# Kernel optimization log

Measured on AMD Instinct MI355X. Metric: run time of the kernel, lower is better.

The kernel has to match this reference:

```python
import jax, jax.numpy as jnp
import numpy as np

B, S, D_FF = 2, 2048, 1024
NUM_HEADS, D_KV = 16, 64
INNER = NUM_HEADS * D_KV


def setup_inputs() -> dict:
    key = jax.random.key(0)
    ks = jax.random.split(key, 8)
    scale = 1.0 / np.sqrt(D_FF)
    return {
        "q": jax.random.normal(ks[0], (B, S, D_FF), jnp.float32),
        "k": jax.random.normal(ks[1], (B, S, D_FF), jnp.float32),
        "v": jax.random.normal(ks[2], (B, S, D_FF), jnp.float32),
        "attn_mask": jax.random.normal(ks[3], (B, 1, S, S), jnp.float32),
        "Wq": jax.random.normal(ks[4], (INNER, D_FF), jnp.float32) * scale,
        "Wk": jax.random.normal(ks[5], (INNER, D_FF), jnp.float32) * scale,
        "Wv": jax.random.normal(ks[6], (INNER, D_FF), jnp.float32) * scale,
        "Wo": jax.random.normal(ks[7], (D_FF, INNER), jnp.float32) * scale,
        "num_heads": NUM_HEADS,
    }


def reference(q, k, v, attn_mask, Wq, Wk, Wv, Wo, num_heads):
    b, s, _ = q.shape
    # torch Linear (no bias): x @ W.T with W of shape [out, in]
    def proj_heads(x, W):
        y = jnp.einsum("bsd,ed->bse", x, W)  # [B,S,inner]
        return y.reshape(b, s, num_heads, -1).transpose(0, 2, 1, 3)  # [B,H,S,dk]

    qh = proj_heads(q, Wq)
    kh = proj_heads(k, Wk)
    vh = proj_heads(v, Wv)
    # T5 attention: NO 1/sqrt(d) scaling; additive mask bias before softmax
    scores = jnp.einsum("bhqd,bhkd->bhqk", qh, kh) + attn_mask  # [B,H,S,S]
    probs = jax.nn.softmax(scores, axis=-1)
    ctx = jnp.einsum("bhqk,bhkd->bhqd", probs, vh)  # [B,H,S,dk]
    ctx = ctx.transpose(0, 2, 1, 3).reshape(b, s, -1)  # [B,S,inner]
    return jnp.einsum("bse,de->bsd", ctx, Wo)  # [B,S,d_ff]
```

## Files before the change

### kernel.cpp

```cpp
#include <hip/hip_runtime.h>
#include <hip/hip_bf16.h>


typedef __attribute__((ext_vector_type(8))) short short8_t;
typedef __attribute__((ext_vector_type(4))) short short4_t;
typedef __attribute__((ext_vector_type(4))) float f32x4_t;

#define SEQ 2048
#define HEADS 16
#define DK 64
#define DFF 1024

__device__ __forceinline__ unsigned short f32_to_bf16(float f) {
  unsigned int u = __float_as_uint(f);
  u += 0x7FFFu + ((u >> 16) & 1u);
  return (unsigned short)(u >> 16);
}
__device__ __forceinline__ float bf16_to_f32(unsigned short h) {
  return __uint_as_float(((unsigned int)h) << 16);
}

__device__ __forceinline__ void gload_lds16(const void* g, void* l) {
  __builtin_amdgcn_global_load_lds(
      (__attribute__((address_space(1))) void*)(g),
      (__attribute__((address_space(3))) void*)(l), 16, 0, 0);
}

__global__ void cvt_x_kernel(const float* __restrict__ q,
                             const float* __restrict__ k,
                             const float* __restrict__ v,
                             short* __restrict__ dst, int n) {
  const float* src = (blockIdx.y == 0) ? q : (blockIdx.y == 1) ? k : v;
  short* out = dst + (size_t)blockIdx.y * n;
  int i = (blockIdx.x * 256 + threadIdx.x) * 4;
  if (i >= n) return;
  float4 f = *(const float4*)(src + i);
  short4_t s;
  s[0] = (short)f32_to_bf16(f.x);
  s[1] = (short)f32_to_bf16(f.y);
  s[2] = (short)f32_to_bf16(f.z);
  s[3] = (short)f32_to_bf16(f.w);
  *(short4_t*)(out + i) = s;
}

__global__ void cvt_w_kernel(const float* __restrict__ Wq,
                             const float* __restrict__ Wk,
                             const float* __restrict__ Wv,
                             const float* __restrict__ Wo,
                             short* __restrict__ wbase, int n) {
  int y = blockIdx.y;
  const float* src = (y == 0) ? Wq : (y == 1) ? Wk : (y == 2) ? Wv : Wo;
  int i = (blockIdx.x * 256 + threadIdx.x) * 4;
  if (i >= n) return;
  float4 f = *(const float4*)(src + i);
  float ff[4] = {f.x, f.y, f.z, f.w};
  if (y < 3) {
    short* hi = wbase + (size_t)(2 * y) * n;
    short* lo = wbase + (size_t)(2 * y + 1) * n;
    short4_t h, l;
#pragma unroll
    for (int j = 0; j < 4; ++j) {
      unsigned short hh = f32_to_bf16(ff[j]);
      h[j] = (short)hh;
      l[j] = (short)f32_to_bf16(ff[j] - bf16_to_f32(hh));
    }
    *(short4_t*)(hi + i) = h;
    *(short4_t*)(lo + i) = l;
  } else {
    short* out = wbase + (size_t)6 * n;
    short4_t s;
#pragma unroll
    for (int j = 0; j < 4; ++j) s[j] = (short)f32_to_bf16(ff[j]);
    *(short4_t*)(out + i) = s;
  }
}

template <int EPI>
__global__ __launch_bounds__(256, 2) void gemm_proj(
    const short* __restrict__ A, const short* __restrict__ Bh,
    const short* __restrict__ Bl, short* __restrict__ Ohi,
    short* __restrict__ Olo, int M, int K) {
  __shared__ short As[128 * 32];
  __shared__ short Bsh[64 * 32];
  __shared__ short Bsl[64 * 32];

  const int tid = threadIdx.x;
  const int w = tid >> 6, l = tid & 63, g = l >> 4, c = l & 15;
  const int wr = w >> 1, wc = w & 1;
  const int m0 = blockIdx.y * 128, n0 = blockIdx.x * 64;

  f32x4_t acc[4][2] = {};

  for (int k0 = 0; k0 < K; k0 += 32) {
#pragma unroll
    for (int j = 0; j < 2; ++j) {
      int e = (w * 2 + j) * 512 + l * 8;
      int r = e >> 5, cc = e & 31;
      gload_lds16(A + (size_t)(m0 + r) * K + k0 + cc, &As[(w * 2 + j) * 512]);
    }
    {
      int e = w * 512 + l * 8;
      int r = e >> 5, cc = e & 31;
      gload_lds16(Bh + (size_t)(n0 + r) * K + k0 + cc, &Bsh[w * 512]);
      gload_lds16(Bl + (size_t)(n0 + r) * K + k0 + cc, &Bsl[w * 512]);
    }
    __syncthreads();

    short8_t a[4], bh[2], bl[2];
#pragma unroll
    for (int mi = 0; mi < 4; ++mi)
      a[mi] = *(const short8_t*)(&As[(wr * 64 + mi * 16 + c) * 32 + g * 8]);
#pragma unroll
    for (int ni = 0; ni < 2; ++ni) {
      bh[ni] = *(const short8_t*)(&Bsh[(wc * 32 + ni * 16 + c) * 32 + g * 8]);
      bl[ni] = *(const short8_t*)(&Bsl[(wc * 32 + ni * 16 + c) * 32 + g * 8]);
    }
#pragma unroll
    for (int mi = 0; mi < 4; ++mi)
#pragma unroll
      for (int ni = 0; ni < 2; ++ni) {
        acc[mi][ni] = __builtin_amdgcn_mfma_f32_16x16x32_bf16(
            a[mi], bh[ni], acc[mi][ni], 0, 0, 0);
        acc[mi][ni] = __builtin_amdgcn_mfma_f32_16x16x32_bf16(
            a[mi], bl[ni], acc[mi][ni], 0, 0, 0);
      }
    __syncthreads();
  }

#pragma unroll
  for (int mi = 0; mi < 4; ++mi) {
#pragma unroll
    for (int ni = 0; ni < 2; ++ni) {
      int col = n0 + wc * 32 + ni * 16 + c;
      int hh = col >> 6, dd = col & 63;
      if (EPI == 2) {
        int row0 = m0 + wr * 64 + mi * 16 + g * 4;
        int bb = row0 >> 11, ss0 = row0 & 2047;
        short4_t s4;
#pragma unroll
        for (int j = 0; j < 4; ++j) s4[j] = (short)f32_to_bf16(acc[mi][ni][j]);
        *(short4_t*)(&Ohi[(((size_t)bb * HEADS + hh) * DK + dd) * SEQ + ss0]) = s4;
      } else {
#pragma unroll
        for (int j = 0; j < 4; ++j) {
          int row = m0 + wr * 64 + mi * 16 + g * 4 + j;
          int bb = row >> 11, ss = row & 2047;
          size_t idx = (((size_t)bb * HEADS + hh) * SEQ + ss) * DK + dd;
          float x = acc[mi][ni][j];
          unsigned short xh = f32_to_bf16(x);
          Ohi[idx] = (short)xh;
          if (EPI == 0)
            Olo[idx] = (short)f32_to_bf16(x - bf16_to_f32(xh));
        }
      }
    }
  }
}

__global__ __launch_bounds__(256, 2) void gemm_out(
    const short* __restrict__ A, const short* __restrict__ Bw,
    float* __restrict__ O, int M, int K) {
  __shared__ short As[128 * 32];
  __shared__ short Bs[64 * 32];

  const int tid = threadIdx.x;
  const int w = tid >> 6, l = tid & 63, g = l >> 4, c = l & 15;
  const int wr = w >> 1, wc = w & 1;
  const int m0 = blockIdx.y * 128, n0 = blockIdx.x * 64;

  f32x4_t acc[4][2] = {};

  for (int k0 = 0; k0 < K; k0 += 32) {
#pragma unroll
    for (int j = 0; j < 2; ++j) {
      int e = (w * 2 + j) * 512 + l * 8;
      int r = e >> 5, cc = e & 31;
      gload_lds16(A + (size_t)(m0 + r) * K + k0 + cc, &As[(w * 2 + j) * 512]);
    }
    {
      int e = w * 512 + l * 8;
      int r = e >> 5, cc = e & 31;
      gload_lds16(Bw + (size_t)(n0 + r) * K + k0 + cc, &Bs[w * 512]);
    }
    __syncthreads();

    short8_t a[4], b[2];
#pragma unroll
    for (int mi = 0; mi < 4; ++mi)
      a[mi] = *(const short8_t*)(&As[(wr * 64 + mi * 16 + c) * 32 + g * 8]);
#pragma unroll
    for (int ni = 0; ni < 2; ++ni)
      b[ni] = *(const short8_t*)(&Bs[(wc * 32 + ni * 16 + c) * 32 + g * 8]);
#pragma unroll
    for (int mi = 0; mi < 4; ++mi)
#pragma unroll
      for (int ni = 0; ni < 2; ++ni)
        acc[mi][ni] = __builtin_amdgcn_mfma_f32_16x16x32_bf16(
            a[mi], b[ni], acc[mi][ni], 0, 0, 0);
    __syncthreads();
  }

#pragma unroll
  for (int mi = 0; mi < 4; ++mi)
#pragma unroll
    for (int ni = 0; ni < 2; ++ni) {
      int col = n0 + wc * 32 + ni * 16 + c;
#pragma unroll
      for (int j = 0; j < 4; ++j) {
        int row = m0 + wr * 64 + mi * 16 + g * 4 + j;
        O[(size_t)row * DFF + col] = acc[mi][ni][j];
      }
    }
}

__global__ __launch_bounds__(512, 4) void attn_kernel(
    const short* __restrict__ qhh, const short* __restrict__ qhl,
    const short* __restrict__ khh, const short* __restrict__ vt,
    const float* __restrict__ mask, short* __restrict__ ctx) {
  const int bh = blockIdx.x;
  const int b = bh >> 4;
  const int h = bh & 15;
  const int qt = blockIdx.y;
  const int tid = threadIdx.x;
  const int w = tid >> 6, l = tid & 63, g = l >> 4, c = l & 15;

  __shared__ short Khs[64 * 72];
  __shared__ short Vts[64 * 72];
  __shared__ short Ps[8][16 * 72];
  short* psw = &Ps[w][0];

  const int qrow0 = qt * 128 + w * 16;
  const short* Qbh = qhh + ((size_t)bh * SEQ + qrow0) * DK;
  const short* Qbl = qhl + ((size_t)bh * SEQ + qrow0) * DK;
  const short* Kbh = khh + (size_t)bh * SEQ * DK;
  const short* Vb  = vt  + (size_t)bh * DK * SEQ;
  const float* M0  = mask + (size_t)b * SEQ * SEQ + (size_t)(qrow0 + c) * SEQ;

  const int srow = tid >> 3;
  const int scol = (tid & 7) * 8;
  const int sofs = srow * 72 + scol;

  short8_t qfh[2], qfl[2];
#pragma unroll
  for (int ks = 0; ks < 2; ++ks) {
    qfh[ks] = *(const short8_t*)(Qbh + (size_t)c * DK + ks * 32 + g * 8);
    qfl[ks] = *(const short8_t*)(Qbl + (size_t)c * DK + ks * 32 + g * 8);
  }

  short8_t rkh = *(const short8_t*)(Kbh + (size_t)srow * DK + scol);
  short8_t rv  = *(const short8_t*)(Vb  + (size_t)srow * SEQ + scol);
  float4 mpre[4];
#pragma unroll
  for (int ni = 0; ni < 4; ++ni)
    mpre[ni] = *(const float4*)(M0 + ni * 16 + g * 4);

  f32x4_t o[4] = {};
  float mrun = -1e30f;
  float lrun = 0.f;

  for (int kv0 = 0; kv0 < SEQ; kv0 += 64) {
    __syncthreads();
    *(short8_t*)(&Khs[sofs]) = rkh;
    *(short8_t*)(&Vts[sofs]) = rv;
    __syncthreads();

    const int kv1 = kv0 + 64;
    if (kv1 < SEQ) {
      rkh = *(const short8_t*)(Kbh + (size_t)(kv1 + srow) * DK + scol);
      rv  = *(const short8_t*)(Vb  + (size_t)srow * SEQ + kv1 + scol);
    }

    f32x4_t sa[4] = {};
    __builtin_amdgcn_s_setprio(1);
#pragma unroll
    for (int ks = 0; ks < 2; ++ks) {
      short8_t ah[4];
#pragma unroll
      for (int ni = 0; ni < 4; ++ni)
        ah[ni] = *(const short8_t*)(&Khs[(ni * 16 + c) * 72 + ks * 32 + g * 8]);
#pragma unroll
      for (int ni = 0; ni < 4; ++ni) {
        sa[ni] = __builtin_amdgcn_mfma_f32_16x16x32_bf16(
            ah[ni], qfh[ks], sa[ni], 0, 0, 0);
        sa[ni] = __builtin_amdgcn_mfma_f32_16x16x32_bf16(
            ah[ni], qfl[ks], sa[ni], 0, 0, 0);
      }
    }
    __builtin_amdgcn_s_setprio(0);

#pragma unroll
    for (int ni = 0; ni < 4; ++ni) {
      sa[ni][0] += mpre[ni].x;
      sa[ni][1] += mpre[ni].y;
      sa[ni][2] += mpre[ni].z;
      sa[ni][3] += mpre[ni].w;
    }
    if (kv1 < SEQ) {
#pragma unroll
      for (int ni = 0; ni < 4; ++ni)
        mpre[ni] = *(const float4*)(M0 + kv1 + ni * 16 + g * 4);
    }

    {
      float t = sa[0][0];
#pragma unroll
      for (int ni = 0; ni < 4; ++ni)
#pragma unroll
        for (int j = 0; j < 4; ++j) t = fmaxf(t, sa[ni][j]);
      t = fmaxf(t, __shfl_xor(t, 16));
      t = fmaxf(t, __shfl_xor(t, 32));
      float mold = mrun;
      float mnew = fmaxf(mold, t);
      float sc = __expf(mold - mnew);
      mrun = mnew;
#pragma unroll
      for (int di = 0; di < 4; ++di)
#pragma unroll
        for (int j = 0; j < 4; ++j) o[di][j] *= sc;
      float psum = 0.f;
#pragma unroll
      for (int ni = 0; ni < 4; ++ni) {
        short4_t ph;
#pragma unroll
        for (int j = 0; j < 4; ++j) {
          float p = __expf(sa[ni][j] - mnew);
          psum += p;
          ph[j] = (short)f32_to_bf16(p);
        }
        *(short4_t*)(&psw[c * 72 + ni * 16 + g * 4]) = ph;
      }
      lrun = lrun * sc + psum;
    }

    __builtin_amdgcn_s_setprio(1);
#pragma unroll
    for (int ks = 0; ks < 2; ++ks) {
      short8_t pb = *(const short8_t*)(&psw[c * 72 + ks * 32 + g * 8]);
#pragma unroll
      for (int di = 0; di < 4; ++di) {
        short8_t av = *(const short8_t*)(&Vts[(di * 16 + c) * 72 + ks * 32 + g * 8]);
        o[di] = __builtin_amdgcn_mfma_f32_16x16x32_bf16(
            av, pb, o[di], 0, 0, 0);
      }
    }
    __builtin_amdgcn_s_setprio(0);
  }

  float s = lrun;
  s += __shfl_xor(s, 16);
  s += __shfl_xor(s, 32);
  float inv = 1.f / s;
  short* Cb = ctx + ((size_t)b * SEQ + qrow0) * DFF + h * DK;
#pragma unroll
  for (int di = 0; di < 4; ++di) {
    short4_t s4;
#pragma unroll
    for (int j = 0; j < 4; ++j)
      s4[j] = (short)f32_to_bf16(o[di][j] * inv);
    *(short4_t*)(Cb + (size_t)c * DFF + di * 16 + g * 4) = s4;
  }
}

extern "C" void kernel_launch(void* const* d_in, const int* in_sizes, int n_in,
                              void* d_out, int out_size, void* d_ws, size_t ws_size,
                              hipStream_t stream) {
  const float* q    = (const float*)d_in[0];
  const float* k    = (const float*)d_in[1];
  const float* v    = (const float*)d_in[2];
  const float* mask = (const float*)d_in[3];
  const float* Wq   = (const float*)d_in[4];
  const float* Wk   = (const float*)d_in[5];
  const float* Wv   = (const float*)d_in[6];
  const float* Wo   = (const float*)d_in[7];
  float* out = (float*)d_out;

  const size_t NQ = 4194304;
  const size_t NW = 1048576;
  short* ws   = (short*)d_ws;
  short* qbf  = ws;
  short* kbf  = ws + NQ;
  short* vbf  = ws + 2 * NQ;
  short* qh_h = ws + 3 * NQ;
  short* qh_l = ws + 4 * NQ;
  short* wbase = ws + 5 * NQ;
  short* wq_h = wbase;
  short* wq_l = wbase + NW;
  short* wk_h = wbase + 2 * NW;
  short* wk_l = wbase + 3 * NW;
  short* wv_h = wbase + 4 * NW;
  short* wv_l = wbase + 5 * NW;
  short* wob  = wbase + 6 * NW;

  short* kh_h = qbf;
  short* vtp  = kbf;
  short* ctx  = vbf;

  cvt_x_kernel<<<dim3(4096, 3), 256, 0, stream>>>(q, k, v, ws, (int)NQ);
  cvt_w_kernel<<<dim3(1024, 4), 256, 0, stream>>>(Wq, Wk, Wv, Wo, wbase, (int)NW);

  dim3 gg(16, 32);
  gemm_proj<0><<<gg, 256, 0, stream>>>(qbf, wq_h, wq_l, qh_h, qh_l, 4096, 1024);
  gemm_proj<1><<<gg, 256, 0, stream>>>(kbf, wk_h, wk_l, kh_h, nullptr, 4096, 1024);
  gemm_proj<2><<<gg, 256, 0, stream>>>(vbf, wv_h, wv_l, vtp, nullptr, 4096, 1024);

  attn_kernel<<<dim3(32, 16), 512, 0, stream>>>(qh_h, qh_l, kh_h, vtp, mask, ctx);

  gemm_out<<<gg, 256, 0, stream>>>(ctx, wob, out, 4096, 1024);
}
```

Measured before the change: 203.1 us.

## Use exp2 softmax with lazy rescaling, packed bf16 convert, and padded LDS stride

Folds log2(e) into the Q projection epilogue and the mask add so the softmax can use exp2f directly. The running-max rescale of the output accumulators is skipped unless some row's max grows by more than 8 (log2 units), which removes most per-tile rescale multiplies. Probabilities are packed to bf16 with a hardware pk convert, replacing manual rounding. The LDS row stride changes from 72 to 76 to alter bank mapping, which risks misaligning the 16-byte LDS loads, and the lazy rescale allows probabilities up to 2^8 before normalisation.

```diff
diff --git a/kernel.cpp b/kernel.cpp
--- a/kernel.cpp
+++ b/kernel.cpp
@@ -10,6 +10,8 @@
 #define HEADS 16
 #define DK 64
 #define DFF 1024
+#define LOG2E 1.44269504088896340736f
+#define LSTR 76
 
 __device__ __forceinline__ unsigned short f32_to_bf16(float f) {
   unsigned int u = __float_as_uint(f);
@@ -18,6 +20,11 @@
 }
 __device__ __forceinline__ float bf16_to_f32(unsigned short h) {
   return __uint_as_float(((unsigned int)h) << 16);
+}
+__device__ __forceinline__ unsigned int cvt_pk_bf16(float a, float b) {
+  unsigned int r;
+  asm("v_cvt_pk_bf16_f32 %0, %1, %2" : "=v"(r) : "v"(a), "v"(b));
+  return r;
 }
 
 __device__ __forceinline__ void gload_lds16(const void* g, void* l) {
@@ -147,6 +154,7 @@
           int bb = row >> 11, ss = row & 2047;
           size_t idx = (((size_t)bb * HEADS + hh) * SEQ + ss) * DK + dd;
           float x = acc[mi][ni][j];
+          if (EPI == 0) x *= LOG2E;
           unsigned short xh = f32_to_bf16(x);
           Ohi[idx] = (short)xh;
           if (EPI == 0)
@@ -224,9 +232,9 @@
   const int tid = threadIdx.x;
   const int w = tid >> 6, l = tid & 63, g = l >> 4, c = l & 15;
 
-  __shared__ short Khs[64 * 72];
-  __shared__ short Vts[64 * 72];
-  __shared__ short Ps[8][16 * 72];
+  __shared__ short Khs[64 * LSTR];
+  __shared__ short Vts[64 * LSTR];
+  __shared__ short Ps[8][16 * LSTR];
   short* psw = &Ps[w][0];
 
   const int qrow0 = qt * 128 + w * 16;
@@ -238,7 +246,7 @@
 
   const int srow = tid >> 3;
   const int scol = (tid & 7) * 8;
-  const int sofs = srow * 72 + scol;
+  const int sofs = srow * LSTR + scol;
 
   short8_t qfh[2], qfl[2];
 #pragma unroll
@@ -274,26 +282,23 @@
     __builtin_amdgcn_s_setprio(1);
 #pragma unroll
     for (int ks = 0; ks < 2; ++ks) {
-      short8_t ah[4];
-#pragma unroll
-      for (int ni = 0; ni < 4; ++ni)
-        ah[ni] = *(const short8_t*)(&Khs[(ni * 16 + c) * 72 + ks * 32 + g * 8]);
 #pragma unroll
       for (int ni = 0; ni < 4; ++ni) {
+        short8_t ah = *(const short8_t*)(&Khs[(ni * 16 + c) * LSTR + ks * 32 + g * 8]);
         sa[ni] = __builtin_amdgcn_mfma_f32_16x16x32_bf16(
-            ah[ni], qfh[ks], sa[ni], 0, 0, 0);
+            ah, qfh[ks], sa[ni], 0, 0, 0);
         sa[ni] = __builtin_amdgcn_mfma_f32_16x16x32_bf16(
-            ah[ni], qfl[ks], sa[ni], 0, 0, 0);
+            ah, qfl[ks], sa[ni], 0, 0, 0);
       }
     }
     __builtin_amdgcn_s_setprio(0);
 
 #pragma unroll
     for (int ni = 0; ni < 4; ++ni) {
-      sa[ni][0] += mpre[ni].x;
-      sa[ni][1] += mpre[ni].y;
-      sa[ni][2] += mpre[ni].z;
-      sa[ni][3] += mpre[ni].w;
+      sa[ni][0] = fmaf(mpre[ni].x, LOG2E, sa[ni][0]);
+      sa[ni][1] = fmaf(mpre[ni].y, LOG2E, sa[ni][1]);
+      sa[ni][2] = fmaf(mpre[ni].z, LOG2E, sa[ni][2]);
+      sa[ni][3] = fmaf(mpre[ni].w, LOG2E, sa[ni][3]);
     }
     if (kv1 < SEQ) {
 #pragma unroll
@@ -309,36 +314,39 @@
         for (int j = 0; j < 4; ++j) t = fmaxf(t, sa[ni][j]);
       t = fmaxf(t, __shfl_xor(t, 16));
       t = fmaxf(t, __shfl_xor(t, 32));
-      float mold = mrun;
-      float mnew = fmaxf(mold, t);
-      float sc = __expf(mold - mnew);
-      mrun = mnew;
-#pragma unroll
-      for (int di = 0; di < 4; ++di)
-#pragma unroll
-        for (int j = 0; j < 4; ++j) o[di][j] *= sc;
+      if (!__all(t - mrun <= 8.f)) {
+        float mnew = fmaxf(mrun, t);
+        float sc = exp2f(mrun - mnew);
+        mrun = mnew;
+        lrun *= sc;
+#pragma unroll
+        for (int di = 0; di < 4; ++di)
+#pragma unroll
+          for (int j = 0; j < 4; ++j) o[di][j] *= sc;
+      }
       float psum = 0.f;
 #pragma unroll
       for (int ni = 0; ni < 4; ++ni) {
-        short4_t ph;
-#pragma unroll
-        for (int j = 0; j < 4; ++j) {
-          float p = __expf(sa[ni][j] - mnew);
-          psum += p;
-          ph[j] = (short)f32_to_bf16(p);
-        }
-        *(short4_t*)(&psw[c * 72 + ni * 16 + g * 4]) = ph;
-      }
-      lrun = lrun * sc + psum;
+        float p0 = exp2f(sa[ni][0] - mrun);
+        float p1 = exp2f(sa[ni][1] - mrun);
+        float p2 = exp2f(sa[ni][2] - mrun);
+        float p3 = exp2f(sa[ni][3] - mrun);
+        psum += (p0 + p1) + (p2 + p3);
+        unsigned int u0 = cvt_pk_bf16(p0, p1);
+        unsigned int u1 = cvt_pk_bf16(p2, p3);
+        unsigned long long pu = ((unsigned long long)u1 << 32) | u0;
+        *(unsigned long long*)(&psw[c * LSTR + ni * 16 + g * 4]) = pu;
+      }
+      lrun += psum;
     }
 
     __builtin_amdgcn_s_setprio(1);
 #pragma unroll
     for (int ks = 0; ks < 2; ++ks) {
-      short8_t pb = *(const short8_t*)(&psw[c * 72 + ks * 32 + g * 8]);
+      short8_t pb = *(const short8_t*)(&psw[c * LSTR + ks * 32 + g * 8]);
 #pragma unroll
       for (int di = 0; di < 4; ++di) {
-        short8_t av = *(const short8_t*)(&Vts[(di * 16 + c) * 72 + ks * 32 + g * 8]);
+        short8_t av = *(const short8_t*)(&Vts[(di * 16 + c) * LSTR + ks * 32 + g * 8]);
         o[di] = __builtin_amdgcn_mfma_f32_16x16x32_bf16(
             av, pb, o[di], 0, 0, 0);
       }
```

New measurement: 215.0 us. 5.9% more time.
